# Kernel optimization log

Hardware: AMD Instinct MI355X
Metric: run time of the kernel (lower is better)

## Reference

```python
import jax, jax.numpy as jnp
import numpy as np

INPUT_SIZE = 512
HIDDEN_SIZE = 4096
OUTPUT_SIZE = 1024
BATCH = 8192


def _xavier_uniform(key, shape):
    fan_out, fan_in = shape
    limit = jnp.sqrt(6.0 / (fan_in + fan_out)).astype(jnp.float32)
    return jax.random.uniform(key, shape, jnp.float32, -limit, limit)


def setup_inputs() -> dict:
    key = jax.random.key(0)
    kx, kk, kg = jax.random.split(key, 3)
    x = jax.random.normal(kx, (BATCH, INPUT_SIZE), dtype=jnp.float32)
    kohonen_weights = _xavier_uniform(kk, (HIDDEN_SIZE, INPUT_SIZE))
    grossberg_weights = _xavier_uniform(kg, (OUTPUT_SIZE, HIDDEN_SIZE))
    return {"x": x, "kohonen_weights": kohonen_weights, "grossberg_weights": grossberg_weights}


def reference(x, kohonen_weights, grossberg_weights):
    x2 = jnp.sum(x * x, axis=1, keepdims=True)                 # [B,1]
    w2 = jnp.sum(kohonen_weights * kohonen_weights, axis=1)    # [H]
    sq = x2 + w2[None, :] - 2.0 * (x @ kohonen_weights.T)      # [B,H]
    distances = jnp.sqrt(jnp.maximum(sq, 0.0))
    winner_indices = jnp.argmin(distances, axis=1)             # [B]
    # one-hot @ grossberg_weights.T == row gather of grossberg columns
    winner_one_hot = jax.nn.one_hot(winner_indices, HIDDEN_SIZE, dtype=x.dtype)  # [B,H]
    output = winner_one_hot @ grossberg_weights.T              # [B,O]
    return (output, winner_indices)
```

## Files before the change

kernel.cpp:

```cpp
#include <hip/hip_runtime.h>
#include <hip/hip_bf16.h>
#include <math.h>

#define BATCH 8192
#define HID   4096
#define KDIM  512
#define OUT   1024

#define BM     128
#define BK     16
#define PAD    132
#define NCHUNK 8
#define CHUNKW 512
#define NSUB   4

__device__ __forceinline__ void top2_upd(float v, int idx, float& v1, int& i1,
                                         float& v2, int& i2) {
  if (v < v1 || (v == v1 && idx < i1)) { v2 = v1; i2 = i1; v1 = v; i1 = idx; }
  else if (v < v2 || (v == v2 && idx < i2)) { v2 = v; i2 = idx; }
}

__global__ void __launch_bounds__(64)
w2_kernel(const float* __restrict__ W, float* __restrict__ w2) {
  int j = blockIdx.x, lane = threadIdx.x;
  const float4* row = (const float4*)(W + (size_t)j * KDIM);
  float s = 0.f;
#pragma unroll
  for (int i = 0; i < 2; ++i) {
    float4 v = row[lane + i * 64];
    s += v.x * v.x + v.y * v.y + v.z * v.z + v.w * v.w;
  }
#pragma unroll
  for (int off = 32; off; off >>= 1) s += __shfl_down(s, off);
  if (lane == 0) w2[j] = s;
}

__global__ void __launch_bounds__(256)
dist_argmin_kernel(const float* __restrict__ X, const float* __restrict__ W,
                   const float* __restrict__ w2, float4* __restrict__ partials) {
  __shared__ float xs[BK][PAD];
  __shared__ float ws_[BK][PAD];

  const int tid = threadIdx.x;
  const int tx = tid & 15, ty = tid >> 4;
  const int rb = blockIdx.x >> 3, chunk = blockIdx.x & 7;
  const int row0 = rb * BM;
  const int col0 = chunk * CHUNKW;

  float v1[8], v2[8];
  int i1[8], i2[8];
#pragma unroll
  for (int i = 0; i < 8; ++i) { v1[i] = v2[i] = 3.4e38f; i1[i] = i2[i] = 0x7fffffff; }

  for (int st = 0; st < NSUB; ++st) {
    const int cbase = col0 + st * BM;
    float acc[8][8];
#pragma unroll
    for (int i = 0; i < 8; ++i)
#pragma unroll
      for (int j = 0; j < 8; ++j) acc[i][j] = 0.f;

    for (int k0 = 0; k0 < KDIM; k0 += BK) {
#pragma unroll
      for (int h = 0; h < 2; ++h) {
        int t = tid + h * 256;
        int r = t >> 2;
        int kk = (t & 3) * 4;
        float4 xv = *(const float4*)(X + (size_t)(row0 + r) * KDIM + k0 + kk);
        xs[kk + 0][r] = xv.x; xs[kk + 1][r] = xv.y;
        xs[kk + 2][r] = xv.z; xs[kk + 3][r] = xv.w;
        float4 wv = *(const float4*)(W + (size_t)(cbase + r) * KDIM + k0 + kk);
        ws_[kk + 0][r] = wv.x; ws_[kk + 1][r] = wv.y;
        ws_[kk + 2][r] = wv.z; ws_[kk + 3][r] = wv.w;
      }
      __syncthreads();
#pragma unroll
      for (int kk = 0; kk < BK; ++kk) {
        float4 a0 = *(const float4*)&xs[kk][ty * 8];
        float4 a1 = *(const float4*)&xs[kk][ty * 8 + 4];
        float4 b0 = *(const float4*)&ws_[kk][tx * 8];
        float4 b1 = *(const float4*)&ws_[kk][tx * 8 + 4];
        float a[8], b[8];
        a[0] = a0.x; a[1] = a0.y; a[2] = a0.z; a[3] = a0.w;
        a[4] = a1.x; a[5] = a1.y; a[6] = a1.z; a[7] = a1.w;
        b[0] = b0.x; b[1] = b0.y; b[2] = b0.z; b[3] = b0.w;
        b[4] = b1.x; b[5] = b1.y; b[6] = b1.z; b[7] = b1.w;
#pragma unroll
        for (int i = 0; i < 8; ++i)
#pragma unroll
          for (int j = 0; j < 8; ++j)
            acc[i][j] = fmaf(a[i], b[j], acc[i][j]);
      }
      __syncthreads();
    }
#pragma unroll
    for (int j = 0; j < 8; ++j) {
      int col = cbase + tx * 8 + j;
      float w2c = w2[col];
#pragma unroll
      for (int i = 0; i < 8; ++i) {
        float v = fmaf(-2.f, acc[i][j], w2c);
        top2_upd(v, col, v1[i], i1[i], v2[i], i2[i]);
      }
    }
  }

#pragma unroll
  for (int m = 1; m < 16; m <<= 1) {
#pragma unroll
    for (int i = 0; i < 8; ++i) {
      float ov1 = __shfl_xor(v1[i], m);
      float ov2 = __shfl_xor(v2[i], m);
      int oi1 = __shfl_xor(i1[i], m);
      int oi2 = __shfl_xor(i2[i], m);
      top2_upd(ov1, oi1, v1[i], i1[i], v2[i], i2[i]);
      top2_upd(ov2, oi2, v1[i], i1[i], v2[i], i2[i]);
    }
  }
  if (tx == 0) {
#pragma unroll
    for (int i = 0; i < 8; ++i) {
      partials[(size_t)(row0 + ty * 8 + i) * NCHUNK + chunk] =
          make_float4(v1[i], v2[i], __int_as_float(i1[i]), __int_as_float(i2[i]));
    }
  }
}

__global__ void __launch_bounds__(256)
recheck_kernel(const float* __restrict__ X, const float* __restrict__ W,
               const float4* __restrict__ partials, int* __restrict__ win,
               float* __restrict__ out_idx) {
  int lane = threadIdx.x & 63;
  int b = blockIdx.x * 4 + (threadIdx.x >> 6);
  float bv1 = 3.4e38f, bv2 = 3.4e38f;
  int bi1 = 0x7fffffff, bi2 = 0x7fffffff;
#pragma unroll
  for (int c = 0; c < NCHUNK; ++c) {
    float4 p = partials[(size_t)b * NCHUNK + c];
    top2_upd(p.x, __float_as_int(p.z), bv1, bi1, bv2, bi2);
    top2_upd(p.y, __float_as_int(p.w), bv1, bi1, bv2, bi2);
  }
  const float* xr  = X + (size_t)b * KDIM;
  const float* wr1 = W + (size_t)bi1 * KDIM;
  const float* wr2 = W + (size_t)bi2 * KDIM;
  double s1 = 0.0, s2 = 0.0;
#pragma unroll
  for (int i = 0; i < KDIM / 64; ++i) {
    int k = lane + i * 64;
    double xv = (double)xr[k];
    double d1 = xv - (double)wr1[k];
    double d2 = xv - (double)wr2[k];
    s1 += d1 * d1;
    s2 += d2 * d2;
  }
#pragma unroll
  for (int off = 32; off; off >>= 1) {
    s1 += __shfl_down(s1, off);
    s2 += __shfl_down(s2, off);
  }
  if (lane == 0) {
    int wi = (s2 < s1 || (s2 == s1 && bi2 < bi1)) ? bi2 : bi1;
    win[b] = wi;
    out_idx[b] = (float)wi;
  }
}

__global__ void __launch_bounds__(256)
gather_kernel(const float* __restrict__ G, const int* __restrict__ win,
              float* __restrict__ out0) {
  int b = blockIdx.x;
  int w = win[b];
  w = (w < 0) ? 0 : (w > HID - 1 ? HID - 1 : w);
#pragma unroll
  for (int i = 0; i < OUT / 256; ++i) {
    int o = threadIdx.x + i * 256;
    out0[(size_t)b * OUT + o] = G[(size_t)o * HID + w];
  }
}

extern "C" void kernel_launch(void* const* d_in, const int* in_sizes, int n_in,
                              void* d_out, int out_size, void* d_ws, size_t ws_size,
                              hipStream_t stream) {
  const float* X = (const float*)d_in[0];
  const float* W = (const float*)d_in[1];
  const float* G = (const float*)d_in[2];
  float* out0 = (float*)d_out;
  float* out_idx = out0 + (size_t)BATCH * OUT;

  char* ws = (char*)d_ws;
  float* w2 = (float*)ws;
  float4* partials = (float4*)(ws + 16 * 1024);
  int* win = (int*)(ws + 16 * 1024 + (size_t)BATCH * NCHUNK * 16);

  w2_kernel<<<HID, 64, 0, stream>>>(W, w2);
  dist_argmin_kernel<<<512, 256, 0, stream>>>(X, W, w2, partials);
  recheck_kernel<<<BATCH / 4, 256, 0, stream>>>(X, W, partials, win, out_idx);
  gather_kernel<<<BATCH, 256, 0, stream>>>(G, win, out0);
}
```

Before: 778.7 us.

## Compute distance GEMM with split-bf16 MFMA and top-3 exact recheck

The scalar FP32 distance GEMM is replaced with matrix-core MFMA. X and W are each split into bf16 hi and lo parts, and three bf16 products are accumulated to approximate FP32 precision. Partial top-2 results per 64-column chunk feed a recheck that recomputes the top-3 candidates exactly in double, which guards against the reduced precision. This adds split passes and more partials traffic, and the gather now writes vectorised float4 stores.

```diff
diff --git a/kernel.cpp b/kernel.cpp
--- a/kernel.cpp
+++ b/kernel.cpp
@@ -7,17 +7,48 @@
 #define KDIM  512
 #define OUT   1024
 
-#define BM     128
-#define BK     16
-#define PAD    132
-#define NCHUNK 8
-#define CHUNKW 512
-#define NSUB   4
+#define BM 128
+#define BN 128
+#define BK 32
+#define NKSTEP (KDIM / BK)
+#define NCH 64
+
+typedef __attribute__((ext_vector_type(8))) short bf16x8;
+typedef __attribute__((ext_vector_type(4))) float f32x4;
+
+__device__ __forceinline__ ushort bf16_rne(float x) {
+  unsigned u = __float_as_uint(x);
+  unsigned r = u + 0x7fffu + ((u >> 16) & 1u);
+  return (ushort)(r >> 16);
+}
 
 __device__ __forceinline__ void top2_upd(float v, int idx, float& v1, int& i1,
                                          float& v2, int& i2) {
   if (v < v1 || (v == v1 && idx < i1)) { v2 = v1; i2 = i1; v1 = v; i1 = idx; }
   else if (v < v2 || (v == v2 && idx < i2)) { v2 = v; i2 = idx; }
+}
+
+__device__ __forceinline__ void top3_upd(float v, int idx,
+    float& v1, int& i1, float& v2, int& i2, float& v3, int& i3) {
+  if (v < v1 || (v == v1 && idx < i1)) { v3 = v2; i3 = i2; v2 = v1; i2 = i1; v1 = v; i1 = idx; }
+  else if (v < v2 || (v == v2 && idx < i2)) { v3 = v2; i3 = i2; v2 = v; i2 = idx; }
+  else if (v < v3 || (v == v3 && idx < i3)) { v3 = v; i3 = idx; }
+}
+
+__global__ void __launch_bounds__(256)
+split_kernel(const float* __restrict__ src, ushort* __restrict__ hi,
+             ushort* __restrict__ lo, int n4) {
+  int i = blockIdx.x * 256 + threadIdx.x;
+  if (i >= n4) return;
+  float4 v = ((const float4*)src)[i];
+  ushort4 h, l;
+  float f;
+  h.x = bf16_rne(v.x); f = __uint_as_float((unsigned)h.x << 16); l.x = bf16_rne(v.x - f);
+  h.y = bf16_rne(v.y); f = __uint_as_float((unsigned)h.y << 16); l.y = bf16_rne(v.y - f);
+  h.z = bf16_rne(v.z); f = __uint_as_float((unsigned)h.z << 16); l.z = bf16_rne(v.z - f);
+  h.w = bf16_rne(v.w); f = __uint_as_float((unsigned)h.w << 16); l.w = bf16_rne(v.w - f);
+  ((ushort4*)hi)[i] = h;
+  ((ushort4*)lo)[i] = l;
 }
 
 __global__ void __launch_bounds__(64)
@@ -36,93 +67,141 @@
 }
 
 __global__ void __launch_bounds__(256)
-dist_argmin_kernel(const float* __restrict__ X, const float* __restrict__ W,
-                   const float* __restrict__ w2, float4* __restrict__ partials) {
-  __shared__ float xs[BK][PAD];
-  __shared__ float ws_[BK][PAD];
+mfma_dist_kernel(const ushort* __restrict__ xh, const ushort* __restrict__ xl,
+                 const ushort* __restrict__ wh, const ushort* __restrict__ wl,
+                 const float* __restrict__ w2, float4* __restrict__ partials) {
+  __shared__ ushort xh_s[4 * 128 * 8];
+  __shared__ ushort xl_s[4 * 128 * 8];
+  __shared__ ushort wh_s[4 * 128 * 8];
+  __shared__ ushort wl_s[4 * 128 * 8];
 
   const int tid = threadIdx.x;
-  const int tx = tid & 15, ty = tid >> 4;
-  const int rb = blockIdx.x >> 3, chunk = blockIdx.x & 7;
+  const int wg = (int)blockIdx.x;
+  const int swz = (wg & 7) * 256 + (wg >> 3);
+  const int rb = swz >> 5;
+  const int cb = swz & 31;
   const int row0 = rb * BM;
-  const int col0 = chunk * CHUNKW;
-
-  float v1[8], v2[8];
-  int i1[8], i2[8];
-#pragma unroll
-  for (int i = 0; i < 8; ++i) { v1[i] = v2[i] = 3.4e38f; i1[i] = i2[i] = 0x7fffffff; }
-
-  for (int st = 0; st < NSUB; ++st) {
-    const int cbase = col0 + st * BM;
-    float acc[8][8];
-#pragma unroll
-    for (int i = 0; i < 8; ++i)
-#pragma unroll
-      for (int j = 0; j < 8; ++j) acc[i][j] = 0.f;
-
-    for (int k0 = 0; k0 < KDIM; k0 += BK) {
-#pragma unroll
-      for (int h = 0; h < 2; ++h) {
-        int t = tid + h * 256;
-        int r = t >> 2;
-        int kk = (t & 3) * 4;
-        float4 xv = *(const float4*)(X + (size_t)(row0 + r) * KDIM + k0 + kk);
-        xs[kk + 0][r] = xv.x; xs[kk + 1][r] = xv.y;
-        xs[kk + 2][r] = xv.z; xs[kk + 3][r] = xv.w;
-        float4 wv = *(const float4*)(W + (size_t)(cbase + r) * KDIM + k0 + kk);
-        ws_[kk + 0][r] = wv.x; ws_[kk + 1][r] = wv.y;
-        ws_[kk + 2][r] = wv.z; ws_[kk + 3][r] = wv.w;
-      }
-      __syncthreads();
-#pragma unroll
-      for (int kk = 0; kk < BK; ++kk) {
-        float4 a0 = *(const float4*)&xs[kk][ty * 8];
-        float4 a1 = *(const float4*)&xs[kk][ty * 8 + 4];
-        float4 b0 = *(const float4*)&ws_[kk][tx * 8];
-        float4 b1 = *(const float4*)&ws_[kk][tx * 8 + 4];
-        float a[8], b[8];
-        a[0] = a0.x; a[1] = a0.y; a[2] = a0.z; a[3] = a0.w;
-        a[4] = a1.x; a[5] = a1.y; a[6] = a1.z; a[7] = a1.w;
-        b[0] = b0.x; b[1] = b0.y; b[2] = b0.z; b[3] = b0.w;
-        b[4] = b1.x; b[5] = b1.y; b[6] = b1.z; b[7] = b1.w;
-#pragma unroll
-        for (int i = 0; i < 8; ++i)
-#pragma unroll
-          for (int j = 0; j < 8; ++j)
-            acc[i][j] = fmaf(a[i], b[j], acc[i][j]);
-      }
-      __syncthreads();
+  const int col0 = cb * BN;
+
+  const int skb = tid & 3;
+  const int sr = tid >> 2;
+  const size_t gx0 = (size_t)(row0 + sr) * KDIM + skb * 8;
+  const size_t gx1 = (size_t)(row0 + sr + 64) * KDIM + skb * 8;
+  const size_t gw0 = (size_t)(col0 + sr) * KDIM + skb * 8;
+  const size_t gw1 = (size_t)(col0 + sr + 64) * KDIM + skb * 8;
+  const int su0 = (skb * 128 + sr) * 8;
+  const int su1 = (skb * 128 + sr + 64) * 8;
+
+  const int lane = tid & 63;
+  const int wid = tid >> 6;
+  const int wr = wid >> 1, wc = wid & 1;
+  const int lr = lane & 15, lg = lane >> 4;
+
+  f32x4 acc[4][4];
+#pragma unroll
+  for (int mi = 0; mi < 4; ++mi)
+#pragma unroll
+    for (int ni = 0; ni < 4; ++ni) acc[mi][ni] = (f32x4){0.f, 0.f, 0.f, 0.f};
+
+  uint4 rxh0, rxh1, rxl0, rxl1, rwh0, rwh1, rwl0, rwl1;
+  rxh0 = *(const uint4*)(xh + gx0); rxh1 = *(const uint4*)(xh + gx1);
+  rxl0 = *(const uint4*)(xl + gx0); rxl1 = *(const uint4*)(xl + gx1);
+  rwh0 = *(const uint4*)(wh + gw0); rwh1 = *(const uint4*)(wh + gw1);
+  rwl0 = *(const uint4*)(wl + gw0); rwl1 = *(const uint4*)(wl + gw1);
+
+  for (int step = 0; step < NKSTEP; ++step) {
+    __syncthreads();
+    *(uint4*)&xh_s[su0] = rxh0; *(uint4*)&xh_s[su1] = rxh1;
+    *(uint4*)&xl_s[su0] = rxl0; *(uint4*)&xl_s[su1] = rxl1;
+    *(uint4*)&wh_s[su0] = rwh0; *(uint4*)&wh_s[su1] = rwh1;
+    *(uint4*)&wl_s[su0] = rwl0; *(uint4*)&wl_s[su1] = rwl1;
+    __syncthreads();
+
+    if (step + 1 < NKSTEP) {
+      const int k1 = (step + 1) * BK;
+      rxh0 = *(const uint4*)(xh + gx0 + k1); rxh1 = *(const uint4*)(xh + gx1 + k1);
+      rxl0 = *(const uint4*)(xl + gx0 + k1); rxl1 = *(const uint4*)(xl + gx1 + k1);
+      rwh0 = *(const uint4*)(wh + gw0 + k1); rwh1 = *(const uint4*)(wh + gw1 + k1);
+      rwl0 = *(const uint4*)(wl + gw0 + k1); rwl1 = *(const uint4*)(wl + gw1 + k1);
     }
-#pragma unroll
-    for (int j = 0; j < 8; ++j) {
-      int col = cbase + tx * 8 + j;
-      float w2c = w2[col];
-#pragma unroll
-      for (int i = 0; i < 8; ++i) {
-        float v = fmaf(-2.f, acc[i][j], w2c);
-        top2_upd(v, col, v1[i], i1[i], v2[i], i2[i]);
+
+    const int abase = (lg * 128 + wr * 64 + lr) * 8;
+    const int bbase = (lg * 128 + wc * 64 + lr) * 8;
+    bf16x8 af[4], al[4], bfr[4];
+#pragma unroll
+    for (int mi = 0; mi < 4; ++mi) af[mi] = *(const bf16x8*)&xh_s[abase + mi * 128];
+#pragma unroll
+    for (int mi = 0; mi < 4; ++mi) al[mi] = *(const bf16x8*)&xl_s[abase + mi * 128];
+#pragma unroll
+    for (int ni = 0; ni < 4; ++ni) bfr[ni] = *(const bf16x8*)&wh_s[bbase + ni * 128];
+#pragma unroll
+    for (int mi = 0; mi < 4; ++mi)
+#pragma unroll
+      for (int ni = 0; ni < 4; ++ni)
+        acc[mi][ni] = __builtin_amdgcn_mfma_f32_16x16x32_bf16(af[mi], bfr[ni], acc[mi][ni], 0, 0, 0);
+#pragma unroll
+    for (int mi = 0; mi < 4; ++mi)
+#pragma unroll
+      for (int ni = 0; ni < 4; ++ni)
+        acc[mi][ni] = __builtin_amdgcn_mfma_f32_16x16x32_bf16(al[mi], bfr[ni], acc[mi][ni], 0, 0, 0);
+#pragma unroll
+    for (int ni = 0; ni < 4; ++ni) bfr[ni] = *(const bf16x8*)&wl_s[bbase + ni * 128];
+#pragma unroll
+    for (int mi = 0; mi < 4; ++mi)
+#pragma unroll
+      for (int ni = 0; ni < 4; ++ni)
+        acc[mi][ni] = __builtin_amdgcn_mfma_f32_16x16x32_bf16(af[mi], bfr[ni], acc[mi][ni], 0, 0, 0);
+  }
+
+  float w2v[4];
+#pragma unroll
+  for (int ni = 0; ni < 4; ++ni) w2v[ni] = w2[col0 + wc * 64 + ni * 16 + lr];
+
+  float v1[4][4], v2[4][4];
+  int i1[4][4], i2[4][4];
+#pragma unroll
+  for (int mi = 0; mi < 4; ++mi)
+#pragma unroll
+    for (int rg = 0; rg < 4; ++rg) {
+      v1[mi][rg] = 3.4e38f; v2[mi][rg] = 3.4e38f;
+      i1[mi][rg] = 0x7fffffff; i2[mi][rg] = 0x7fffffff;
+    }
+#pragma unroll
+  for (int mi = 0; mi < 4; ++mi)
+#pragma unroll
+    for (int ni = 0; ni < 4; ++ni) {
+      const int col = col0 + wc * 64 + ni * 16 + lr;
+#pragma unroll
+      for (int rg = 0; rg < 4; ++rg) {
+        float v = fmaf(-2.f, acc[mi][ni][rg], w2v[ni]);
+        top2_upd(v, col, v1[mi][rg], i1[mi][rg], v2[mi][rg], i2[mi][rg]);
       }
     }
-  }
-
 #pragma unroll
   for (int m = 1; m < 16; m <<= 1) {
 #pragma unroll
-    for (int i = 0; i < 8; ++i) {
-      float ov1 = __shfl_xor(v1[i], m);
-      float ov2 = __shfl_xor(v2[i], m);
-      int oi1 = __shfl_xor(i1[i], m);
-      int oi2 = __shfl_xor(i2[i], m);
-      top2_upd(ov1, oi1, v1[i], i1[i], v2[i], i2[i]);
-      top2_upd(ov2, oi2, v1[i], i1[i], v2[i], i2[i]);
-    }
-  }
-  if (tx == 0) {
-#pragma unroll
-    for (int i = 0; i < 8; ++i) {
-      partials[(size_t)(row0 + ty * 8 + i) * NCHUNK + chunk] =
-          make_float4(v1[i], v2[i], __int_as_float(i1[i]), __int_as_float(i2[i]));
-    }
+    for (int mi = 0; mi < 4; ++mi)
+#pragma unroll
+      for (int rg = 0; rg < 4; ++rg) {
+        float ov1 = __shfl_xor(v1[mi][rg], m);
+        int oi1 = __shfl_xor(i1[mi][rg], m);
+        float ov2 = __shfl_xor(v2[mi][rg], m);
+        int oi2 = __shfl_xor(i2[mi][rg], m);
+        top2_upd(ov1, oi1, v1[mi][rg], i1[mi][rg], v2[mi][rg], i2[mi][rg]);
+        top2_upd(ov2, oi2, v1[mi][rg], i1[mi][rg], v2[mi][rg], i2[mi][rg]);
+      }
+  }
+  if (lr == 0) {
+    const int chunk = cb * 2 + wc;
+#pragma unroll
+    for (int mi = 0; mi < 4; ++mi)
+#pragma unroll
+      for (int rg = 0; rg < 4; ++rg) {
+        const int row = row0 + wr * 64 + mi * 16 + lg * 4 + rg;
+        partials[(size_t)row * NCH + chunk] =
+            make_float4(v1[mi][rg], v2[mi][rg],
+                        __int_as_float(i1[mi][rg]), __int_as_float(i2[mi][rg]));
+      }
   }
 }
 
@@ -132,34 +211,37 @@
                float* __restrict__ out_idx) {
   int lane = threadIdx.x & 63;
   int b = blockIdx.x * 4 + (threadIdx.x >> 6);
-  float bv1 = 3.4e38f, bv2 = 3.4e38f;
-  int bi1 = 0x7fffffff, bi2 = 0x7fffffff;
-#pragma unroll
-  for (int c = 0; c < NCHUNK; ++c) {
-    float4 p = partials[(size_t)b * NCHUNK + c];
-    top2_upd(p.x, __float_as_int(p.z), bv1, bi1, bv2, bi2);
-    top2_upd(p.y, __float_as_int(p.w), bv1, bi1, bv2, bi2);
-  }
-  const float* xr  = X + (size_t)b * KDIM;
-  const float* wr1 = W + (size_t)bi1 * KDIM;
-  const float* wr2 = W + (size_t)bi2 * KDIM;
-  double s1 = 0.0, s2 = 0.0;
+  float v1 = 3.4e38f, v2 = 3.4e38f, v3 = 3.4e38f;
+  int i1 = 0x7fffffff, i2 = 0x7fffffff, i3 = 0x7fffffff;
+  for (int c = 0; c < NCH; ++c) {
+    float4 p = partials[(size_t)b * NCH + c];
+    top3_upd(p.x, __float_as_int(p.z), v1, i1, v2, i2, v3, i3);
+    top3_upd(p.y, __float_as_int(p.w), v1, i1, v2, i2, v3, i3);
+  }
+  const float* xr = X + (size_t)b * KDIM;
+  const float* w1 = W + (size_t)i1 * KDIM;
+  const float* w2p = W + (size_t)i2 * KDIM;
+  const float* w3 = W + (size_t)i3 * KDIM;
+  double s1 = 0.0, s2 = 0.0, s3 = 0.0;
 #pragma unroll
   for (int i = 0; i < KDIM / 64; ++i) {
     int k = lane + i * 64;
     double xv = (double)xr[k];
-    double d1 = xv - (double)wr1[k];
-    double d2 = xv - (double)wr2[k];
-    s1 += d1 * d1;
-    s2 += d2 * d2;
+    double d1 = xv - (double)w1[k];
+    double d2 = xv - (double)w2p[k];
+    double d3 = xv - (double)w3[k];
+    s1 += d1 * d1; s2 += d2 * d2; s3 += d3 * d3;
   }
 #pragma unroll
   for (int off = 32; off; off >>= 1) {
     s1 += __shfl_down(s1, off);
     s2 += __shfl_down(s2, off);
+    s3 += __shfl_down(s3, off);
   }
   if (lane == 0) {
-    int wi = (s2 < s1 || (s2 == s1 && bi2 < bi1)) ? bi2 : bi1;
+    int wi = i1; double sb = s1;
+    if (s2 < sb || (s2 == sb && i2 < wi)) { sb = s2; wi = i2; }
+    if (s3 < sb || (s3 == sb && i3 < wi)) { sb = s3; wi = i3; }
     win[b] = wi;
     out_idx[b] = (float)wi;
   }
@@ -171,11 +253,13 @@
   int b = blockIdx.x;
   int w = win[b];
   w = (w < 0) ? 0 : (w > HID - 1 ? HID - 1 : w);
-#pragma unroll
-  for (int i = 0; i < OUT / 256; ++i) {
-    int o = threadIdx.x + i * 256;
-    out0[(size_t)b * OUT + o] = G[(size_t)o * HID + w];
-  }
+  int o = threadIdx.x * 4;
+  float4 r;
+  r.x = G[(size_t)(o + 0) * HID + w];
+  r.y = G[(size_t)(o + 1) * HID + w];
+  r.z = G[(size_t)(o + 2) * HID + w];
+  r.w = G[(size_t)(o + 3) * HID + w];
+  *(float4*)&out0[(size_t)b * OUT + o] = r;
 }
 
 extern "C" void kernel_launch(void* const* d_in, const int* in_sizes, int n_in,
@@ -189,11 +273,17 @@
 
   char* ws = (char*)d_ws;
   float* w2 = (float*)ws;
-  float4* partials = (float4*)(ws + 16 * 1024);
-  int* win = (int*)(ws + 16 * 1024 + (size_t)BATCH * NCHUNK * 16);
-
+  int* win = (int*)(ws + 16384);
+  float4* partials = (float4*)(ws + 65536);
+  ushort* xh = (ushort*)(ws + 65536 + 8388608);
+  ushort* xl = xh + (size_t)BATCH * KDIM;
+  ushort* wh = xl + (size_t)BATCH * KDIM;
+  ushort* wl = wh + (size_t)HID * KDIM;
+
+  split_kernel<<<4096, 256, 0, stream>>>(X, xh, xl, BATCH * KDIM / 4);
+  split_kernel<<<2048, 256, 0, stream>>>(W, wh, wl, HID * KDIM / 4);
   w2_kernel<<<HID, 64, 0, stream>>>(W, w2);
-  dist_argmin_kernel<<<512, 256, 0, stream>>>(X, W, w2, partials);
+  mfma_dist_kernel<<<2048, 256, 0, stream>>>(xh, xl, wh, wl, w2, partials);
   recheck_kernel<<<BATCH / 4, 256, 0, stream>>>(X, W, partials, win, out_idx);
   gather_kernel<<<BATCH, 256, 0, stream>>>(G, win, out0);
 }
```

Measured after the change: 905.7 us. 1.16x slower.
